# Kernel optimization log

Hardware: AMD Instinct MI355X
Metric: run time of the kernel (lower is better)

The kernel has to match this reference:

```python
import jax, jax.numpy as jnp
import numpy as np

B, L, F_DIM, H = 4, 384, 640, 128
K_COULOMB = 332.0
DIELECTRIC = 80.0
BN_EPS = 1e-5

# amino-acid charge table, index order 'ACDEFGHIKLMNPQRSTVWY'
_AA = 'ACDEFGHIKLMNPQRSTVWY'
_CHG = {'D': -1.0, 'E': -1.0, 'K': 1.0, 'R': 1.0, 'H': 0.1}
_TABLE = np.zeros((20, 3), dtype=np.float32)
for _i, _aa in enumerate(_AA):
    c = _CHG.get(_aa, 0.0)
    _TABLE[_i, 0 if c > 0 else (1 if c < 0 else 2)] = 1.0
CHG_TABLE = jnp.asarray(_TABLE)


def _conv1d(x, w, b, pad):
    # x: [N, Cin, L], w: [Cout, Cin, K]
    y = jax.lax.conv_general_dilated(x, w, (1,), [(pad, pad)],
                                     dimension_numbers=('NCH', 'OIH', 'NCH'))
    return y + b[None, :, None]


def setup_inputs() -> dict:
    key = jax.random.key(0)
    ks = jax.random.split(key, 32)
    s = 0.05

    def rn(k, shape):
        return (jax.random.normal(k, shape) * s).astype(jnp.float32)

    inp = {
        'features': jax.random.normal(ks[0], (B, L, F_DIM), dtype=jnp.float32),
        'seq_ids': jax.random.randint(ks[1], (B, L), 0, 20, dtype=jnp.int32),
        'structures': (jax.random.normal(ks[2], (B, L, 3)) * 10.0).astype(jnp.float32),
        # charge predictor: Linear(F,H) -> ReLU -> BN(H) -> Linear(H,H//2) -> ReLU -> Linear(H//2,3) -> Softmax
        'W1': rn(ks[3], (F_DIM, H)), 'b1': jnp.zeros((H,), jnp.float32),
        'gamma': jnp.ones((H,), jnp.float32), 'beta': jnp.zeros((H,), jnp.float32),
        'rmean': jnp.zeros((H,), jnp.float32), 'rvar': jnp.ones((H,), jnp.float32),
        'W2': rn(ks[4], (H, H // 2)), 'b2': jnp.zeros((H // 2,), jnp.float32),
        'W3': rn(ks[5], (H // 2, 3)), 'b3': jnp.zeros((3,), jnp.float32),
        # salt bridge detector: Linear(2F+1,H) -> ReLU -> Linear(H,64) -> ReLU -> Linear(64,1) -> Sigmoid
        'sW1': rn(ks[6], (2 * F_DIM + 1, H)), 'sb1': jnp.zeros((H,), jnp.float32),
        'sW2': rn(ks[7], (H, 64)), 'sb2': jnp.zeros((64,), jnp.float32),
        'sW3': rn(ks[8], (64, 1)), 'sb3': jnp.zeros((1,), jnp.float32),
        # potential calculator convs (OIH layout)
        'c1w': rn(ks[9], (16, 1, 5)), 'c1b': jnp.zeros((16,), jnp.float32),
        'c2w': rn(ks[10], (8, 16, 3)), 'c2b': jnp.zeros((8,), jnp.float32),
        'c3w': rn(ks[11], (1, 8, 3)), 'c3b': jnp.zeros((1,), jnp.float32),
    }
    return inp


def reference(features, seq_ids, structures,
              W1, b1, gamma, beta, rmean, rvar, W2, b2, W3, b3,
              sW1, sb1, sW2, sb2, sW3, sb3,
              c1w, c1b, c2w, c2b, c3w, c3b):
    b_, l_, f_ = features.shape

    # true charges from sequence (one-hot pos/neg/neutral)
    true_charges = CHG_TABLE[seq_ids]                               # [B,L,3]

    # --- charge predictor (BatchNorm in eval mode: running stats) ---
    x = features.reshape(-1, f_)
    h = jax.nn.relu(x @ W1 + b1)
    h = gamma * (h - rmean) / jnp.sqrt(rvar + BN_EPS) + beta
    h = jax.nn.relu(h @ W2 + b2)
    pc = jax.nn.softmax(h @ W3 + b3, axis=-1).reshape(b_, l_, 3)    # [B,L,3]

    net_charge = pc[:, :, 0:1] - pc[:, :, 1:2]                      # [B,L,1]

    # --- electrostatic potential: 1D conv stack on [B,1,L] ---
    p = net_charge.transpose(0, 2, 1)                               # [B,1,L]
    p = jax.nn.relu(_conv1d(p, c1w, c1b, 2))
    p = jax.nn.relu(_conv1d(p, c2w, c2b, 1))
    p = _conv1d(p, c3w, c3b, 1)
    potential = p.transpose(0, 2, 1)                                # [B,L,1]

    # --- pairwise distances ---
    diff = structures[:, :, None, :] - structures[:, None, :, :]    # [B,L,L,3]
    D = jnp.sqrt(jnp.sum(diff * diff, axis=-1) + 1e-12)             # [B,L,L]

    # --- salt bridges: vectorized edge-MLP over all (pos i, neg j) pairs ---
    pos = pc[:, :, 0] > pc[:, :, 2]                                 # [B,L]
    neg = pc[:, :, 1] > pc[:, :, 2]                                 # [B,L]
    a, bb, d = sW1[:f_], sW1[f_:2 * f_], sW1[2 * f_]                # split cat([fi,fj,dist]) @ sW1
    fi = features @ a                                               # [B,L,H]
    fj = features @ bb                                              # [B,L,H]
    hid = jax.nn.relu(fi[:, :, None, :] + fj[:, None, :, :] + D[..., None] * d + sb1)  # [B,L,L,H]
    hid2 = jax.nn.relu(hid @ sW2 + sb2)                             # [B,L,L,64]
    prob = jax.nn.sigmoid((hid2 @ sW3 + sb3)[..., 0])               # [B,L,L]
    q = pos[:, :, None] & neg[:, None, :] & (D < 4.0) & (prob > 0.5)
    salt_bridge_masks = (q | q.transpose(0, 2, 1)).astype(jnp.float32)  # [B,L,L]

    # --- Coulomb energy with distance-dependent dielectric ---
    # dielectric = eps * D / 4 -> e_ij = k * q_i q_j / (eps/4 * D^2)
    qc = pc[:, :, 0] - pc[:, :, 1]                                  # [B,L]
    valid = (D < 15.0) & (D > 0.0)
    triu = jnp.triu(jnp.ones((l_, l_), bool), k=1)[None]
    D_safe = jnp.where(valid, D, 1.0)
    e_ij = K_COULOMB * qc[:, :, None] * qc[:, None, :] / ((DIELECTRIC / 4.0) * D_safe * D_safe)
    energy = jnp.sum(jnp.where(valid & triu, e_ij, 0.0), axis=(1, 2))  # [B]

    return (pc, true_charges, net_charge, potential, salt_bridge_masks, energy)
```

## Files before the change

kernel.cpp:

```cpp
#include <hip/hip_runtime.h>

#define LSEQ 384
#define NROWS 1536
#define FDIM 640
#define HDIM 128
#define PART 196608

#define WS_H1P 0
#define WS_FIP (4*PART)
#define WS_FJP (8*PART)
#define WS_FI  (12*PART)
#define WS_FJ  (13*PART)
#define WS_QC  (14*PART)
#define WS_FLAG (WS_QC + NROWS)
#define WS_EPART (WS_FLAG + NROWS)
#define WS_DONE  (WS_EPART + 384)

#define OUT_PC    0
#define OUT_TC    4608
#define OUT_NET   9216
#define OUT_POT   10752
#define OUT_MASK  12288
#define OUT_EN    602112

__global__ __launch_bounds__(256) void k_gemm(const float* __restrict__ X,
                                              const float* __restrict__ W1,
                                              const float* __restrict__ sW1,
                                              float* __restrict__ ws) {
    __shared__ float As[2 * 32 * 34];
    __shared__ float Bs[2 * 32 * 64];
    const int t = threadIdx.x;
    if (blockIdx.x == 0 && blockIdx.y == 0 && blockIdx.z == 0) {
        for (int idx = t; idx < 385; idx += 256)
            ws[WS_EPART + idx] = 0.0f;
    }

    const int m0 = blockIdx.x * 32;
    const int gy = blockIdx.y, kz = blockIdx.z;
    const int mat = gy >> 1, half = gy & 1, n0 = half * 64;
    const float* W = (mat == 0) ? W1 : (mat == 1 ? sW1 : sW1 + 640 * 128);
    float* O = ws + (mat == 0 ? WS_H1P : (mat == 1 ? WS_FIP : WS_FJP)) + kz * PART;

    const int a_r = t >> 3, a_c = (t & 7) * 4;
    const int b_r = t >> 4, b_c = (t & 15) * 4;
    const int tx = (t & 15) * 4, ty = (t >> 4) * 2;
    const int k0 = kz * 160;

    float acc[2][4] = {};

    float4 av  = *(const float4*)&X[(m0 + a_r) * FDIM + k0 + a_c];
    float4 bv0 = *(const float4*)&W[(k0 + b_r) * HDIM + n0 + b_c];
    float4 bv1 = *(const float4*)&W[(k0 + b_r + 16) * HDIM + n0 + b_c];
    As[(a_c + 0) * 34 + a_r] = av.x;
    As[(a_c + 1) * 34 + a_r] = av.y;
    As[(a_c + 2) * 34 + a_r] = av.z;
    As[(a_c + 3) * 34 + a_r] = av.w;
    *(float4*)&Bs[b_r * 64 + b_c]        = bv0;
    *(float4*)&Bs[(b_r + 16) * 64 + b_c] = bv1;
    __syncthreads();

    for (int it = 0; it < 5; it++) {
        const int buf = it & 1;
        if (it < 4) {
            const int kk = k0 + (it + 1) * 32;
            av  = *(const float4*)&X[(m0 + a_r) * FDIM + kk + a_c];
            bv0 = *(const float4*)&W[(kk + b_r) * HDIM + n0 + b_c];
            bv1 = *(const float4*)&W[(kk + b_r + 16) * HDIM + n0 + b_c];
        }
        const float* Ab = As + buf * 1088;
        const float* Bb = Bs + buf * 2048;
#pragma unroll
        for (int k = 0; k < 32; k++) {
            float2 a = *(const float2*)&Ab[k * 34 + ty];
            float4 b = *(const float4*)&Bb[k * 64 + tx];
            acc[0][0] = fmaf(a.x, b.x, acc[0][0]);
            acc[0][1] = fmaf(a.x, b.y, acc[0][1]);
            acc[0][2] = fmaf(a.x, b.z, acc[0][2]);
            acc[0][3] = fmaf(a.x, b.w, acc[0][3]);
            acc[1][0] = fmaf(a.y, b.x, acc[1][0]);
            acc[1][1] = fmaf(a.y, b.y, acc[1][1]);
            acc[1][2] = fmaf(a.y, b.z, acc[1][2]);
            acc[1][3] = fmaf(a.y, b.w, acc[1][3]);
        }
        if (it < 4) {
            float* Aw = As + (buf ^ 1) * 1088;
            float* Bw = Bs + (buf ^ 1) * 2048;
            Aw[(a_c + 0) * 34 + a_r] = av.x;
            Aw[(a_c + 1) * 34 + a_r] = av.y;
            Aw[(a_c + 2) * 34 + a_r] = av.z;
            Aw[(a_c + 3) * 34 + a_r] = av.w;
            *(float4*)&Bw[b_r * 64 + b_c]        = bv0;
            *(float4*)&Bw[(b_r + 16) * 64 + b_c] = bv1;
            __syncthreads();
        }
    }
#pragma unroll
    for (int r = 0; r < 2; r++) {
        float4 v = make_float4(acc[r][0], acc[r][1], acc[r][2], acc[r][3]);
        *(float4*)&O[(m0 + ty + r) * HDIM + n0 + tx] = v;
    }
}

__global__ __launch_bounds__(256) void k_row(float* __restrict__ ws,
                                             const float* __restrict__ b1,
                                             const float* __restrict__ gam,
                                             const float* __restrict__ bet,
                                             const float* __restrict__ rmean,
                                             const float* __restrict__ rvar,
                                             const float* __restrict__ W2,
                                             const float* __restrict__ b2,
                                             const float* __restrict__ W3,
                                             const float* __restrict__ b3,
                                             const int* __restrict__ seq,
                                             float* __restrict__ out) {
    const int t = threadIdx.x, w = t >> 6, lane = t & 63;
    const int row = blockIdx.x * 4 + w;
    const long base = (long)row * 128;
    const float* h1p = ws + WS_H1P;
    const float* fip = ws + WS_FIP;
    const float* fjp = ws + WS_FJP;

    {
        float fi0 = fip[base + lane] + fip[PART + base + lane]
                  + fip[2 * PART + base + lane] + fip[3 * PART + base + lane];
        float fi1 = fip[base + 64 + lane] + fip[PART + base + 64 + lane]
                  + fip[2 * PART + base + 64 + lane] + fip[3 * PART + base + 64 + lane];
        float fj0 = fjp[base + lane] + fjp[PART + base + lane]
                  + fjp[2 * PART + base + lane] + fjp[3 * PART + base + lane];
        float fj1 = fjp[base + 64 + lane] + fjp[PART + base + 64 + lane]
                  + fjp[2 * PART + base + 64 + lane] + fjp[3 * PART + base + 64 + lane];
        ws[WS_FI + base + lane]      = fi0;
        ws[WS_FI + base + 64 + lane] = fi1;
        ws[WS_FJ + base + lane]      = fj0;
        ws[WS_FJ + base + 64 + lane] = fj1;
    }

    float h0 = h1p[base + lane] + h1p[PART + base + lane]
             + h1p[2 * PART + base + lane] + h1p[3 * PART + base + lane];
    float h1 = h1p[base + 64 + lane] + h1p[PART + base + 64 + lane]
             + h1p[2 * PART + base + 64 + lane] + h1p[3 * PART + base + 64 + lane];
    h0 = fmaxf(h0 + b1[lane], 0.0f);
    h1 = fmaxf(h1 + b1[64 + lane], 0.0f);
    h0 = gam[lane]      * (h0 - rmean[lane])      / sqrtf(rvar[lane] + 1e-5f)      + bet[lane];
    h1 = gam[64 + lane] * (h1 - rmean[64 + lane]) / sqrtf(rvar[64 + lane] + 1e-5f) + bet[64 + lane];

    float acc = b2[lane];
#pragma unroll
    for (int cc = 0; cc < 64; cc++) {
        float wv0 = W2[cc * 64 + lane];
        float wv1 = W2[(cc + 64) * 64 + lane];
        float hv0 = __uint_as_float(__builtin_amdgcn_readlane(__float_as_uint(h0), cc));
        float hv1 = __uint_as_float(__builtin_amdgcn_readlane(__float_as_uint(h1), cc));
        acc = fmaf(hv0, wv0, acc);
        acc = fmaf(hv1, wv1, acc);
    }
    float h2 = fmaxf(acc, 0.0f);
    float x0 = h2 * W3[lane * 3 + 0];
    float x1 = h2 * W3[lane * 3 + 1];
    float x2 = h2 * W3[lane * 3 + 2];
#pragma unroll
    for (int o = 32; o > 0; o >>= 1) {
        x0 += __shfl_xor(x0, o, 64);
        x1 += __shfl_xor(x1, o, 64);
        x2 += __shfl_xor(x2, o, 64);
    }
    if (lane == 0) {
        float l0 = x0 + b3[0], l1 = x1 + b3[1], l2 = x2 + b3[2];
        float m = fmaxf(l0, fmaxf(l1, l2));
        float e0 = expf(l0 - m), e1 = expf(l1 - m), e2 = expf(l2 - m);
        float s = e0 + e1 + e2;
        float pc0 = e0 / s, pc1 = e1 / s, pc2 = e2 / s;
        out[OUT_PC + row * 3 + 0] = pc0;
        out[OUT_PC + row * 3 + 1] = pc1;
        out[OUT_PC + row * 3 + 2] = pc2;
        float net = pc0 - pc1;
        out[OUT_NET + row] = net;
        ws[WS_QC + row] = net;
        ((int*)(ws + WS_FLAG))[row] = (pc0 > pc2 ? 1 : 0) | (pc1 > pc2 ? 2 : 0);
        int sid = seq[row];
        float c0 = (sid == 6 || sid == 8 || sid == 14) ? 1.0f : 0.0f;
        float c1 = (sid == 2 || sid == 3) ? 1.0f : 0.0f;
        out[OUT_TC + row * 3 + 0] = c0;
        out[OUT_TC + row * 3 + 1] = c1;
        out[OUT_TC + row * 3 + 2] = (c0 == 0.0f && c1 == 0.0f) ? 1.0f : 0.0f;
    }
}

__device__ __forceinline__ float mlp_eval(const float* __restrict__ fi, const float* __restrict__ fj,
                                          int gi, int gj, float D,
                                          float dv0, float dv1, float sb0, float sb1v,
                                          float b2v, float w3l, const float* __restrict__ sW2, int lane) {
    float h0 = fmaxf(fi[(long)gi * 128 + lane]      + fj[(long)gj * 128 + lane]      + D * dv0 + sb0,  0.0f);
    float h1 = fmaxf(fi[(long)gi * 128 + 64 + lane] + fj[(long)gj * 128 + 64 + lane] + D * dv1 + sb1v, 0.0f);
    float a0 = 0.0f, a1 = 0.0f;
#pragma unroll 8
    for (int cc = 0; cc < 64; cc++) {
        float hv0 = __uint_as_float(__builtin_amdgcn_readlane(__float_as_uint(h0), cc));
        float hv1 = __uint_as_float(__builtin_amdgcn_readlane(__float_as_uint(h1), cc));
        a0 = fmaf(hv0, sW2[cc * 64 + lane], a0);
        a1 = fmaf(hv1, sW2[(cc + 64) * 64 + lane], a1);
    }
    float x = fmaxf(a0 + a1 + b2v, 0.0f) * w3l;
#pragma unroll
    for (int o = 32; o > 0; o >>= 1) x += __shfl_xor(x, o, 64);
    return x;
}

__global__ __launch_bounds__(256, 6) void k2(const float* __restrict__ S,
                                             float* __restrict__ ws,
                                             const float* __restrict__ sW1,
                                             const float* __restrict__ sb1,
                                             const float* __restrict__ sW2,
                                             const float* __restrict__ sb2,
                                             const float* __restrict__ sW3,
                                             const float* __restrict__ sb3,
                                             const float* __restrict__ c1w, const float* __restrict__ c1b,
                                             const float* __restrict__ c2w, const float* __restrict__ c2b,
                                             const float* __restrict__ c3w, const float* __restrict__ c3b,
                                             float* __restrict__ out) {
    __shared__ char smem[8192];
    const int t = threadIdx.x;
    const int bi = blockIdx.x;

    if (bi < 4) {
        float* p0h = (float*)smem;
        const int b = bi;
        for (int idx = t; idx < 392; idx += 256)
            p0h[idx] = (idx >= 4 && idx < 388) ? out[OUT_NET + b * LSEQ + (idx - 4)] : 0.0f;
        __syncthreads();
        for (int pos = t; pos < LSEQ; pos += 256) {
            float p2v[8][3];
#pragma unroll
            for (int o2 = 0; o2 < 8; o2++) {
                float cb = c2b[o2];
#pragma unroll
                for (int d1 = 0; d1 < 3; d1++) p2v[o2][d1] = cb;
            }
            for (int i = 0; i < 16; i++) {
                float p1v[5];
#pragma unroll
                for (int d2 = 0; d2 < 5; d2++) {
                    int q2 = pos - 2 + d2;
                    float a = c1b[i];
#pragma unroll
                    for (int k = 0; k < 5; k++)
                        a = fmaf(p0h[q2 + 2 + k], c1w[i * 5 + k], a);
                    p1v[d2] = (q2 >= 0 && q2 < LSEQ) ? fmaxf(a, 0.0f) : 0.0f;
                }
#pragma unroll
                for (int o2 = 0; o2 < 8; o2++) {
#pragma unroll
                    for (int d1 = 0; d1 < 3; d1++) {
#pragma unroll
                        for (int k = 0; k < 3; k++)
                            p2v[o2][d1] = fmaf(p1v[d1 + k], c2w[(o2 * 16 + i) * 3 + k], p2v[o2][d1]);
                    }
                }
            }
            float acc3 = c3b[0];
#pragma unroll
            for (int o2 = 0; o2 < 8; o2++) {
#pragma unroll
                for (int k = 0; k < 3; k++) {
                    int q1 = pos - 1 + k;
                    float pv = (q1 >= 0 && q1 < LSEQ) ? fmaxf(p2v[o2][k], 0.0f) : 0.0f;
                    acc3 = fmaf(pv, c3w[o2 * 3 + k], acc3);
                }
            }
            out[OUT_POT + b * LSEQ + pos] = acc3;
        }
        return;
    }

    float* sx = (float*)smem;
    float* sy = sx + 384;
    float* sz = sy + 384;
    float* sq = sz + 384;
    unsigned int* clist = (unsigned int*)(sq + 384);
    unsigned char* sf = (unsigned char*)(smem + 7680);
    float* red = (float*)(smem + 8064);
    int* cntL = (int*)(smem + 8080);

    const float* qc = ws + WS_QC;
    const int* flags = (const int*)(ws + WS_FLAG);
    const float* fi = ws + WS_FI;
    const float* fj = ws + WS_FJ;

    const int row = bi - 4;
    const int b = row / LSEQ;
    const int i = row - b * LSEQ;

    for (int j = t; j < LSEQ; j += 256) {
        int g = b * LSEQ + j;
        sx[j] = S[g * 3 + 0];
        sy[j] = S[g * 3 + 1];
        sz[j] = S[g * 3 + 2];
        sq[j] = qc[g];
        sf[j] = (unsigned char)flags[g];
    }
    if (t == 0) *cntL = 0;
    __syncthreads();

    const float six = sx[i], siy = sy[i], siz = sz[i], qi = sq[i];
    const int fli = sf[i];
    const bool posi = (fli & 1) != 0, negi = (fli & 2) != 0;
    const int lane = t & 63, w = t >> 6;
    float esum = 0.0f;
    float* mrow = out + OUT_MASK + (long)row * LSEQ;

    for (int j = t; j < LSEQ; j += 256) {
        float dx = __fsub_rn(six, sx[j]);
        float dy = __fsub_rn(siy, sy[j]);
        float dz = __fsub_rn(siz, sz[j]);
        float d2 = __fadd_rn(__fadd_rn(__fmul_rn(dx, dx), __fmul_rn(dy, dy)), __fmul_rn(dz, dz));
        d2 = __fadd_rn(d2, 1e-12f);
        float D = __fsqrt_rn(d2);
        mrow[j] = 0.0f;
        if (j > i && D < 15.0f && D > 0.0f) {
            float num = __fmul_rn(__fmul_rn(332.0f, qi), sq[j]);
            float den = __fmul_rn(__fmul_rn(20.0f, D), D);
            esum += __fdiv_rn(num, den);
        }
        int flj = sf[j];
        bool near = (D < 4.0f);
        bool need1 = near && posi && ((flj & 2) != 0);
        bool need2 = near && negi && ((flj & 1) != 0);
        if (need1 || need2) {
            int p = atomicAdd(cntL, 1);
            clist[p] = (unsigned int)j | (need1 ? 512u : 0u) | (need2 ? 1024u : 0u);
        }
    }
#pragma unroll
    for (int o = 32; o > 0; o >>= 1) esum += __shfl_xor(esum, o, 64);
    if (lane == 0) red[w] = esum;
    __syncthreads();

    int nc = *cntL;
    float blockE = red[0] + red[1] + red[2] + red[3];

    if (nc > 0) {
        const float* dvec = sW1 + 1280 * 128;
        const float dv0 = dvec[lane], dv1 = dvec[lane + 64];
        const float sb0 = sb1[lane], sb1v = sb1[lane + 64];
        const float w3l = sW3[lane];
        const float b2v = sb2[lane];
        const float b3v = sb3[0];
        for (int c = w; c < nc; c += 4) {
            unsigned int e = clist[c];
            int j = (int)(e & 511u);
            bool need1 = (e & 512u) != 0, need2 = (e & 1024u) != 0;
            float dx = __fsub_rn(six, sx[j]);
            float dy = __fsub_rn(siy, sy[j]);
            float dz = __fsub_rn(siz, sz[j]);
            float d2 = __fadd_rn(__fadd_rn(__fmul_rn(dx, dx), __fmul_rn(dy, dy)), __fmul_rn(dz, dz));
            d2 = __fadd_rn(d2, 1e-12f);
            float D = __fsqrt_rn(d2);
            int gi = row, gj = b * LSEQ + j;
            bool hit = false;
            if (need1) {
                float x = mlp_eval(fi, fj, gi, gj, D, dv0, dv1, sb0, sb1v, b2v, w3l, sW2, lane);
                hit = (x + b3v) > 0.0f;
            }
            if (!hit && need2) {
                float x = mlp_eval(fi, fj, gj, gi, D, dv0, dv1, sb0, sb1v, b2v, w3l, sW2, lane);
                hit = (x + b3v) > 0.0f;
            }
            if (hit && lane == 0) mrow[j] = 1.0f;
        }
    }

    unsigned int old = 0xffffffffu;
    if (t == 0) {
        atomicAdd(&ws[WS_EPART + b * 96 + (i % 96)], blockE);
        __threadfence();
        old = atomicAdd((unsigned int*)&ws[WS_DONE], 1u);
    }
    if (t < 64) {
        old = __shfl(old, 0, 64);
        if (old == (unsigned int)(NROWS - 1)) {
#pragma unroll
            for (int bb = 0; bb < 4; bb++) {
                float s = ws[WS_EPART + bb * 96 + lane];
                if (lane < 32) s += ws[WS_EPART + bb * 96 + 64 + lane];
#pragma unroll
                for (int o = 32; o > 0; o >>= 1) s += __shfl_xor(s, o, 64);
                if (lane == 0) out[OUT_EN + bb] = s;
            }
        }
    }
}

extern "C" void kernel_launch(void* const* d_in, const int* in_sizes, int n_in,
                              void* d_out, int out_size, void* d_ws, size_t ws_size,
                              hipStream_t stream) {
    const float* X     = (const float*)d_in[0];
    const int*   seq   = (const int*)d_in[1];
    const float* S     = (const float*)d_in[2];
    const float* W1    = (const float*)d_in[3];
    const float* b1    = (const float*)d_in[4];
    const float* gam   = (const float*)d_in[5];
    const float* bet   = (const float*)d_in[6];
    const float* rmean = (const float*)d_in[7];
    const float* rvar  = (const float*)d_in[8];
    const float* W2    = (const float*)d_in[9];
    const float* b2    = (const float*)d_in[10];
    const float* W3    = (const float*)d_in[11];
    const float* b3    = (const float*)d_in[12];
    const float* sW1   = (const float*)d_in[13];
    const float* sb1   = (const float*)d_in[14];
    const float* sW2   = (const float*)d_in[15];
    const float* sb2   = (const float*)d_in[16];
    const float* sW3   = (const float*)d_in[17];
    const float* sb3   = (const float*)d_in[18];
    const float* c1w   = (const float*)d_in[19];
    const float* c1b   = (const float*)d_in[20];
    const float* c2w   = (const float*)d_in[21];
    const float* c2b   = (const float*)d_in[22];
    const float* c3w   = (const float*)d_in[23];
    const float* c3b   = (const float*)d_in[24];

    float* out = (float*)d_out;
    float* ws  = (float*)d_ws;

    hipLaunchKernelGGL(k_gemm, dim3(48, 6, 4), dim3(256), 0, stream, X, W1, sW1, ws);
    hipLaunchKernelGGL(k_row, dim3(384), dim3(256), 0, stream,
                       ws, b1, gam, bet, rmean, rvar, W2, b2, W3, b3, seq, out);
    hipLaunchKernelGGL(k2, dim3(1540), dim3(256), 0, stream,
                       S, ws, sW1, sb1, sW2, sb2, sW3, sb3,
                       c1w, c1b, c2w, c2b, c3w, c3b, out);
}
```

Before: 168.7 us.

## Map one wavefront per row in k2 and use ballot-driven salt-bridge evaluation

```diff
diff --git a/kernel.cpp b/kernel.cpp
--- a/kernel.cpp
+++ b/kernel.cpp
@@ -13,8 +13,6 @@
 #define WS_FJ  (13*PART)
 #define WS_QC  (14*PART)
 #define WS_FLAG (WS_QC + NROWS)
-#define WS_EPART (WS_FLAG + NROWS)
-#define WS_DONE  (WS_EPART + 384)
 
 #define OUT_PC    0
 #define OUT_TC    4608
@@ -26,14 +24,13 @@
 __global__ __launch_bounds__(256) void k_gemm(const float* __restrict__ X,
                                               const float* __restrict__ W1,
                                               const float* __restrict__ sW1,
-                                              float* __restrict__ ws) {
+                                              float* __restrict__ ws,
+                                              float* __restrict__ out) {
     __shared__ float As[2 * 32 * 34];
     __shared__ float Bs[2 * 32 * 64];
     const int t = threadIdx.x;
-    if (blockIdx.x == 0 && blockIdx.y == 0 && blockIdx.z == 0) {
-        for (int idx = t; idx < 385; idx += 256)
-            ws[WS_EPART + idx] = 0.0f;
-    }
+    if (blockIdx.x == 0 && blockIdx.y == 0 && blockIdx.z == 0 && t < 4)
+        out[OUT_EN + t] = 0.0f;
 
     const int m0 = blockIdx.x * 32;
     const int gy = blockIdx.y, kz = blockIdx.z;
@@ -206,19 +203,19 @@
     return x;
 }
 
-__global__ __launch_bounds__(256, 6) void k2(const float* __restrict__ S,
-                                             float* __restrict__ ws,
-                                             const float* __restrict__ sW1,
-                                             const float* __restrict__ sb1,
-                                             const float* __restrict__ sW2,
-                                             const float* __restrict__ sb2,
-                                             const float* __restrict__ sW3,
-                                             const float* __restrict__ sb3,
-                                             const float* __restrict__ c1w, const float* __restrict__ c1b,
-                                             const float* __restrict__ c2w, const float* __restrict__ c2b,
-                                             const float* __restrict__ c3w, const float* __restrict__ c3b,
-                                             float* __restrict__ out) {
-    __shared__ char smem[8192];
+__global__ __launch_bounds__(256) void k2(const float* __restrict__ S,
+                                          const float* __restrict__ ws,
+                                          const float* __restrict__ sW1,
+                                          const float* __restrict__ sb1,
+                                          const float* __restrict__ sW2,
+                                          const float* __restrict__ sb2,
+                                          const float* __restrict__ sW3,
+                                          const float* __restrict__ sb3,
+                                          const float* __restrict__ c1w, const float* __restrict__ c1b,
+                                          const float* __restrict__ c2w, const float* __restrict__ c2b,
+                                          const float* __restrict__ c3w, const float* __restrict__ c3b,
+                                          float* __restrict__ out) {
+    __shared__ char smem[6592];
     const int t = threadIdx.x;
     const int bi = blockIdx.x;
 
@@ -276,19 +273,19 @@
     float* sy = sx + 384;
     float* sz = sy + 384;
     float* sq = sz + 384;
-    unsigned int* clist = (unsigned int*)(sq + 384);
-    unsigned char* sf = (unsigned char*)(smem + 7680);
-    float* red = (float*)(smem + 8064);
-    int* cntL = (int*)(smem + 8080);
+    unsigned char* sf = (unsigned char*)(sq + 384);
+    float* red = (float*)(smem + 6544);
+
+    red = (float*)(smem + 6528);
 
     const float* qc = ws + WS_QC;
     const int* flags = (const int*)(ws + WS_FLAG);
     const float* fi = ws + WS_FI;
     const float* fj = ws + WS_FJ;
 
-    const int row = bi - 4;
-    const int b = row / LSEQ;
-    const int i = row - b * LSEQ;
+    const int pb = bi - 4;
+    const int b = pb / 96;
+    const int i0 = (pb % 96) * 4;
 
     for (int j = t; j < LSEQ; j += 256) {
         int g = b * LSEQ + j;
@@ -298,24 +295,32 @@
         sq[j] = qc[g];
         sf[j] = (unsigned char)flags[g];
     }
-    if (t == 0) *cntL = 0;
     __syncthreads();
 
+    const int w = t >> 6, lane = t & 63;
+    const int i = i0 + w;
+    const int row = b * LSEQ + i;
     const float six = sx[i], siy = sy[i], siz = sz[i], qi = sq[i];
     const int fli = sf[i];
     const bool posi = (fli & 1) != 0, negi = (fli & 2) != 0;
-    const int lane = t & 63, w = t >> 6;
+    float* mrow = out + OUT_MASK + (long)row * LSEQ;
+
+    const float* dvec = sW1 + 1280 * 128;
+    const float dv0 = dvec[lane], dv1 = dvec[lane + 64];
+    const float sb0 = sb1[lane], sb1v = sb1[lane + 64];
+    const float w3l = sW3[lane];
+    const float b2v = sb2[lane];
+    const float b3v = sb3[0];
+
     float esum = 0.0f;
-    float* mrow = out + OUT_MASK + (long)row * LSEQ;
-
-    for (int j = t; j < LSEQ; j += 256) {
+    for (int j0 = 0; j0 < LSEQ; j0 += 64) {
+        const int j = j0 + lane;
         float dx = __fsub_rn(six, sx[j]);
         float dy = __fsub_rn(siy, sy[j]);
         float dz = __fsub_rn(siz, sz[j]);
         float d2 = __fadd_rn(__fadd_rn(__fmul_rn(dx, dx), __fmul_rn(dy, dy)), __fmul_rn(dz, dz));
         d2 = __fadd_rn(d2, 1e-12f);
         float D = __fsqrt_rn(d2);
-        mrow[j] = 0.0f;
         if (j > i && D < 15.0f && D > 0.0f) {
             float num = __fmul_rn(__fmul_rn(332.0f, qi), sq[j]);
             float den = __fmul_rn(__fmul_rn(20.0f, D), D);
@@ -325,68 +330,35 @@
         bool near = (D < 4.0f);
         bool need1 = near && posi && ((flj & 2) != 0);
         bool need2 = near && negi && ((flj & 1) != 0);
-        if (need1 || need2) {
-            int p = atomicAdd(cntL, 1);
-            clist[p] = (unsigned int)j | (need1 ? 512u : 0u) | (need2 ? 1024u : 0u);
-        }
+        int pk = (need1 ? 1 : 0) | (need2 ? 2 : 0);
+        unsigned long long mb = __ballot(pk != 0);
+        unsigned long long hitbits = 0ull;
+        while (mb) {
+            int jl = __ffsll((long long)mb) - 1;
+            mb &= mb - 1ull;
+            int pf = __shfl(pk, jl, 64);
+            float Dj = __shfl(D, jl, 64);
+            int gj = b * LSEQ + j0 + jl;
+            bool hit = false;
+            if (pf & 1) {
+                float x = mlp_eval(fi, fj, row, gj, Dj, dv0, dv1, sb0, sb1v, b2v, w3l, sW2, lane);
+                hit = (x + b3v) > 0.0f;
+            }
+            if (!hit && (pf & 2)) {
+                float x = mlp_eval(fi, fj, gj, row, Dj, dv0, dv1, sb0, sb1v, b2v, w3l, sW2, lane);
+                hit = (x + b3v) > 0.0f;
+            }
+            if (hit) hitbits |= (1ull << jl);
+        }
+        mrow[j] = ((hitbits >> lane) & 1ull) ? 1.0f : 0.0f;
     }
 #pragma unroll
     for (int o = 32; o > 0; o >>= 1) esum += __shfl_xor(esum, o, 64);
     if (lane == 0) red[w] = esum;
     __syncthreads();
-
-    int nc = *cntL;
-    float blockE = red[0] + red[1] + red[2] + red[3];
-
-    if (nc > 0) {
-        const float* dvec = sW1 + 1280 * 128;
-        const float dv0 = dvec[lane], dv1 = dvec[lane + 64];
-        const float sb0 = sb1[lane], sb1v = sb1[lane + 64];
-        const float w3l = sW3[lane];
-        const float b2v = sb2[lane];
-        const float b3v = sb3[0];
-        for (int c = w; c < nc; c += 4) {
-            unsigned int e = clist[c];
-            int j = (int)(e & 511u);
-            bool need1 = (e & 512u) != 0, need2 = (e & 1024u) != 0;
-            float dx = __fsub_rn(six, sx[j]);
-            float dy = __fsub_rn(siy, sy[j]);
-            float dz = __fsub_rn(siz, sz[j]);
-            float d2 = __fadd_rn(__fadd_rn(__fmul_rn(dx, dx), __fmul_rn(dy, dy)), __fmul_rn(dz, dz));
-            d2 = __fadd_rn(d2, 1e-12f);
-            float D = __fsqrt_rn(d2);
-            int gi = row, gj = b * LSEQ + j;
-            bool hit = false;
-            if (need1) {
-                float x = mlp_eval(fi, fj, gi, gj, D, dv0, dv1, sb0, sb1v, b2v, w3l, sW2, lane);
-                hit = (x + b3v) > 0.0f;
-            }
-            if (!hit && need2) {
-                float x = mlp_eval(fi, fj, gj, gi, D, dv0, dv1, sb0, sb1v, b2v, w3l, sW2, lane);
-                hit = (x + b3v) > 0.0f;
-            }
-            if (hit && lane == 0) mrow[j] = 1.0f;
-        }
-    }
-
-    unsigned int old = 0xffffffffu;
     if (t == 0) {
-        atomicAdd(&ws[WS_EPART + b * 96 + (i % 96)], blockE);
-        __threadfence();
-        old = atomicAdd((unsigned int*)&ws[WS_DONE], 1u);
-    }
-    if (t < 64) {
-        old = __shfl(old, 0, 64);
-        if (old == (unsigned int)(NROWS - 1)) {
-#pragma unroll
-            for (int bb = 0; bb < 4; bb++) {
-                float s = ws[WS_EPART + bb * 96 + lane];
-                if (lane < 32) s += ws[WS_EPART + bb * 96 + 64 + lane];
-#pragma unroll
-                for (int o = 32; o > 0; o >>= 1) s += __shfl_xor(s, o, 64);
-                if (lane == 0) out[OUT_EN + bb] = s;
-            }
-        }
+        float s = red[0] + red[1] + red[2] + red[3];
+        atomicAdd(&out[OUT_EN + b], s);
     }
 }
 
@@ -422,10 +394,10 @@
     float* out = (float*)d_out;
     float* ws  = (float*)d_ws;
 
-    hipLaunchKernelGGL(k_gemm, dim3(48, 6, 4), dim3(256), 0, stream, X, W1, sW1, ws);
+    hipLaunchKernelGGL(k_gemm, dim3(48, 6, 4), dim3(256), 0, stream, X, W1, sW1, ws, out);
     hipLaunchKernelGGL(k_row, dim3(384), dim3(256), 0, stream,
                        ws, b1, gam, bet, rmean, rvar, W2, b2, W3, b3, seq, out);
-    hipLaunchKernelGGL(k2, dim3(1540), dim3(256), 0, stream,
+    hipLaunchKernelGGL(k2, dim3(388), dim3(256), 0, stream,
                        S, ws, sW1, sb1, sW2, sb2, sW3, sb3,
                        c1w, c1b, c2w, c2b, c3w, c3b, out);
 }
```

Measured after the change: 165.4 us. 1.02x faster.
